# Optimization experiments

Hardware: AMD Instinct MI355X
Metric: run time of the kernel (lower is better)

The kernel has to match this reference:

```python
import jax, jax.numpy as jnp
import numpy as np

TEMPERATURE = 0.1
NEGATIVE_WEIGHT = 1.0
NORM_EPS = 1e-12  # matches torch F.normalize clamp_min eps


def setup_inputs() -> dict:
    key = jax.random.key(0)
    x = jax.random.normal(key, (8, 128, 16, 8, 8), dtype=jnp.float32)
    return {"x": x}


def reference(x):
    B, F, T, H, W = x.shape
    # transpose(0,1).flatten(1).transpose(0,1): (B,F,T,H,W) -> (N, F), N = B*T*H*W
    feats = jnp.transpose(x, (1, 0, 2, 3, 4)).reshape(F, -1).T  # [N, F]
    norms = jnp.maximum(jnp.linalg.norm(feats, axis=1, keepdims=True), NORM_EPS)
    x_norm = feats / norms  # unit vectors, [N, F]
    sims = (x_norm @ x_norm.T) / TEMPERATURE  # [N, N] cosine similarities
    n = sims.shape[0]
    # masked_select(~eye) + logsumexp == logsumexp with diagonal set to -inf
    sims = jnp.where(jnp.eye(n, dtype=bool), -jnp.inf, sims)
    diversity_loss = jax.nn.logsumexp(sims)
    return NEGATIVE_WEIGHT * diversity_loss
```

## Files before the change

### kernel.cpp

```cpp
#include <hip/hip_runtime.h>
#include <hip/hip_fp8.h>
#include <math.h>


#define NTILE 8256
#define NPBLK 1376

typedef __attribute__((ext_vector_type(4))) float f32x4;
typedef __attribute__((ext_vector_type(2))) long i64x2;

#if __has_builtin(__builtin_amdgcn_exp2f)
#define EXP2F(x) __builtin_amdgcn_exp2f(x)
#else
#define EXP2F(x) exp2f(x)
#endif

__device__ inline unsigned int pk_fp8(float f0, float f1, float f2, float f3) {
#if __has_builtin(__builtin_amdgcn_cvt_pk_fp8_f32)
    unsigned int r = 0;
    r = __builtin_amdgcn_cvt_pk_fp8_f32(f0, f1, r, false);
    r = __builtin_amdgcn_cvt_pk_fp8_f32(f2, f3, r, true);
    return r;
#else
    union { unsigned char b[4]; unsigned int u; } v;
    v.b[0] = __hip_fp8_e4m3(f0).__x; v.b[1] = __hip_fp8_e4m3(f1).__x;
    v.b[2] = __hip_fp8_e4m3(f2).__x; v.b[3] = __hip_fp8_e4m3(f3).__x;
    return v.u;
#endif
}

__global__ __launch_bounds__(256)
void normalize_kernel(const float* __restrict__ x, unsigned char* __restrict__ Xs) {
    __shared__ float ldsf[128][33];
    __shared__ float ssred[8][32];
    __shared__ float invs[32];
    const int tid = threadIdx.x;
    const int b  = blockIdx.x >> 5;
    const int r0 = (blockIdx.x & 31) * 32;
    const int rl = tid & 31, fp = tid >> 5;
    const float* px = x + b * 131072 + r0 + rl;
    float ss = 0.f;
#pragma unroll
    for (int j = 0; j < 16; ++j) {
        int f = fp * 16 + j;
        float v = px[f * 1024];
        ldsf[f][rl] = v;
        ss = fmaf(v, v, ss);
    }
    ssred[fp][rl] = ss;
    __syncthreads();
    if (tid < 32) {
        float s = 0.f;
#pragma unroll
        for (int k = 0; k < 8; ++k) s += ssred[k][tid];
        invs[tid] = 1.0f / fmaxf(sqrtf(s), 1e-12f);
    }
    __syncthreads();
    {
        const int c   = tid;
        const int rgl = c >> 7;
        const int cc  = c & 127;
        const int t8  = (cc >> 6) & 1, q = (cc >> 4) & 3, r = cc & 15;
        const int row = rgl * 16 + r;
        const float inv = invs[row];
        union { unsigned int w[4]; int4 v; } u;
#pragma unroll
        for (int half = 0; half < 2; ++half) {
            const int k0 = t8 * 64 + half * 32 + q * 8;
            u.w[half * 2 + 0] = pk_fp8(ldsf[k0 + 0][row] * inv, ldsf[k0 + 1][row] * inv,
                                       ldsf[k0 + 2][row] * inv, ldsf[k0 + 3][row] * inv);
            u.w[half * 2 + 1] = pk_fp8(ldsf[k0 + 4][row] * inv, ldsf[k0 + 5][row] * inv,
                                       ldsf[k0 + 6][row] * inv, ldsf[k0 + 7][row] * inv);
        }
        const int rgg = blockIdx.x * 2 + rgl;
        ((int4*)Xs)[rgg * 128 + cc] = u.v;
    }
}

__global__ __launch_bounds__(256)
void gram_lse_kernel(const i64x2* __restrict__ Xs, float* __restrict__ partials) {
    const int bk = blockIdx.x;
    const int tid = threadIdx.x;
    const int lane = tid & 63, w = tid >> 6;
    const int ga = (w & 1) * 2;
    const int gb = (w >> 1) * 2;
    const int quad = lane >> 4, colL = lane & 15;
    const float C = 14.426950408889634f;

    int L = bk * 6, I0 = 0;
    while (L >= 128 - I0) { L -= 128 - I0; ++I0; }
    int Is[6], Js[6];
    {
        int ii = I0, jj = I0 + L;
#pragma unroll
        for (int s = 0; s < 6; ++s) {
            Is[s] = ii; Js[s] = jj;
            if (++jj == 128) { ++ii; jj = ii; }
        }
    }

    i64x2 av[2][2];
    int IcurA = Is[0];
#pragma unroll
    for (int g = 0; g < 2; ++g)
#pragma unroll
        for (int t8 = 0; t8 < 2; ++t8)
            av[g][t8] = Xs[(Is[0] * 4 + ga + g) * 128 + t8 * 64 + lane];

    float wsum = 0.f;
#pragma unroll
    for (int s = 0; s < 6; ++s) {
        if (Is[s] != IcurA) {
#pragma unroll
            for (int g = 0; g < 2; ++g)
#pragma unroll
                for (int t8 = 0; t8 < 2; ++t8)
                    av[g][t8] = Xs[(Is[s] * 4 + ga + g) * 128 + t8 * 64 + lane];
            IcurA = Is[s];
        }

        i64x2 bv[2][2];
#pragma unroll
        for (int g = 0; g < 2; ++g)
#pragma unroll
            for (int t8 = 0; t8 < 2; ++t8)
                bv[g][t8] = Xs[(Js[s] * 4 + gb + g) * 128 + t8 * 64 + lane];

        f32x4 acc[2][2];
#pragma unroll
        for (int i = 0; i < 2; ++i)
#pragma unroll
            for (int j = 0; j < 2; ++j) acc[i][j] = (f32x4){0.f, 0.f, 0.f, 0.f};
#pragma unroll
        for (int t = 0; t < 4; ++t) {
            const int th = t >> 1, tl = t & 1;
            long aL[2], bL[2];
#pragma unroll
            for (int g = 0; g < 2; ++g) {
                aL[g] = av[g][th][tl];
                bL[g] = bv[g][th][tl];
            }
#pragma unroll
            for (int i = 0; i < 2; ++i)
#pragma unroll
                for (int j = 0; j < 2; ++j)
                    acc[i][j] = __builtin_amdgcn_mfma_f32_16x16x32_fp8_fp8(
                        aL[i], bL[j], acc[i][j], 0, 0, 0);
        }

        const bool diagT = (Is[s] == Js[s]);
        float lsum = 0.f;
#pragma unroll
        for (int i = 0; i < 2; ++i) {
            const int rbase = (ga + i) * 16 + quad * 4;
#pragma unroll
            for (int j = 0; j < 2; ++j) {
                const int cbase = (gb + j) * 16 + colL;
#pragma unroll
                for (int g = 0; g < 4; ++g) {
                    if (diagT && (rbase + g == cbase)) continue;
                    lsum += EXP2F(fmaf(C, acc[i][j][g], -C));
                }
            }
        }
        wsum += diagT ? lsum : 2.0f * lsum;
    }

#pragma unroll
    for (int o = 32; o > 0; o >>= 1) wsum += __shfl_down(wsum, o, 64);
    __shared__ float red[4];
    if (lane == 0) red[w] = wsum;
    __syncthreads();
    if (tid == 0) partials[bk] = red[0] + red[1] + red[2] + red[3];
}

__global__ __launch_bounds__(256)
void final_kernel(const float* __restrict__ partials, float* __restrict__ out) {
    double s = 0.0;
    for (int i = threadIdx.x; i < NPBLK; i += 256) s += (double)partials[i];
#pragma unroll
    for (int o = 32; o > 0; o >>= 1) s += __shfl_down(s, o, 64);
    __shared__ double red[4];
    if ((threadIdx.x & 63) == 0) red[threadIdx.x >> 6] = s;
    __syncthreads();
    if (threadIdx.x == 0)
        out[0] = (float)(10.0 + log(red[0] + red[1] + red[2] + red[3]));
}

extern "C" void kernel_launch(void* const* d_in, const int* in_sizes, int n_in,
                              void* d_out, int out_size, void* d_ws, size_t ws_size,
                              hipStream_t stream) {
    const float* x = (const float*)d_in[0];
    float* out = (float*)d_out;
    float* partials = (float*)d_ws;
    unsigned char* Xs = (unsigned char*)d_ws + 131072;

    normalize_kernel<<<256, 256, 0, stream>>>(x, Xs);
    gram_lse_kernel<<<NPBLK, 256, 0, stream>>>((const i64x2*)Xs, partials);
    final_kernel<<<1, 256, 0, stream>>>(partials, out);
}
```

Before: 72.76 us.

## Stage 128-row macro tile pairs in LDS and reuse across 2x2 sub-tiles

Result: faster. 70.27 us (-3.4%).

```diff
diff --git a/kernel.cpp b/kernel.cpp
--- a/kernel.cpp
+++ b/kernel.cpp
@@ -3,8 +3,7 @@
 #include <math.h>
 
 
-#define NTILE 8256
-#define NPBLK 1376
+#define NMACR 2080
 
 typedef __attribute__((ext_vector_type(4))) float f32x4;
 typedef __attribute__((ext_vector_type(2))) long i64x2;
@@ -87,83 +86,99 @@
     const int quad = lane >> 4, colL = lane & 15;
     const float C = 14.426950408889634f;
 
-    int L = bk * 6, I0 = 0;
-    while (L >= 128 - I0) { L -= 128 - I0; ++I0; }
-    int Is[6], Js[6];
+    int I;
     {
-        int ii = I0, jj = I0 + L;
-#pragma unroll
-        for (int s = 0; s < 6; ++s) {
-            Is[s] = ii; Js[s] = jj;
-            if (++jj == 128) { ++ii; jj = ii; }
+        const int t = bk;
+        I = (int)((129.0 - sqrt(16641.0 - 8.0 * (double)t)) * 0.5);
+        if (I < 0) I = 0;
+        while ((((I + 1) * (128 - I)) >> 1) <= t) ++I;
+        while (((I * (129 - I)) >> 1) > t) --I;
+    }
+    const int J = I + (bk - ((I * (129 - I)) >> 1));
+    const bool diagM = (I == J);
+
+    __shared__ i64x2 ldsA[1024];
+    __shared__ i64x2 ldsB[1024];
+    {
+        const i64x2* pa = Xs + I * 1024;
+        if (diagM) {
+#pragma unroll
+            for (int i = 0; i < 4; ++i)
+                ldsA[tid + i * 256] = pa[tid + i * 256];
+        } else {
+            const i64x2* pb = Xs + J * 1024;
+#pragma unroll
+            for (int i = 0; i < 4; ++i) {
+                ldsA[tid + i * 256] = pa[tid + i * 256];
+                ldsB[tid + i * 256] = pb[tid + i * 256];
+            }
         }
     }
-
-    i64x2 av[2][2];
-    int IcurA = Is[0];
-#pragma unroll
-    for (int g = 0; g < 2; ++g)
-#pragma unroll
-        for (int t8 = 0; t8 < 2; ++t8)
-            av[g][t8] = Xs[(Is[0] * 4 + ga + g) * 128 + t8 * 64 + lane];
+    __syncthreads();
+    const i64x2* lb = diagM ? ldsA : ldsB;
+
+    i64x2 avv[2][2][2];
+#pragma unroll
+    for (int ti = 0; ti < 2; ++ti)
+#pragma unroll
+        for (int g = 0; g < 2; ++g)
+#pragma unroll
+            for (int t8 = 0; t8 < 2; ++t8)
+                avv[ti][g][t8] = ldsA[(ti * 4 + ga + g) * 128 + t8 * 64 + lane];
 
     float wsum = 0.f;
 #pragma unroll
-    for (int s = 0; s < 6; ++s) {
-        if (Is[s] != IcurA) {
-#pragma unroll
-            for (int g = 0; g < 2; ++g)
-#pragma unroll
-                for (int t8 = 0; t8 < 2; ++t8)
-                    av[g][t8] = Xs[(Is[s] * 4 + ga + g) * 128 + t8 * 64 + lane];
-            IcurA = Is[s];
-        }
-
-        i64x2 bv[2][2];
+    for (int tj = 0; tj < 2; ++tj) {
+        i64x2 bvv[2][2];
 #pragma unroll
         for (int g = 0; g < 2; ++g)
 #pragma unroll
             for (int t8 = 0; t8 < 2; ++t8)
-                bv[g][t8] = Xs[(Js[s] * 4 + gb + g) * 128 + t8 * 64 + lane];
-
-        f32x4 acc[2][2];
-#pragma unroll
-        for (int i = 0; i < 2; ++i)
-#pragma unroll
-            for (int j = 0; j < 2; ++j) acc[i][j] = (f32x4){0.f, 0.f, 0.f, 0.f};
-#pragma unroll
-        for (int t = 0; t < 4; ++t) {
-            const int th = t >> 1, tl = t & 1;
-            long aL[2], bL[2];
-#pragma unroll
-            for (int g = 0; g < 2; ++g) {
-                aL[g] = av[g][th][tl];
-                bL[g] = bv[g][th][tl];
+                bvv[g][t8] = lb[(tj * 4 + gb + g) * 128 + t8 * 64 + lane];
+
+#pragma unroll
+        for (int ti = 0; ti < 2; ++ti) {
+            if (diagM && ti > tj) continue;
+            const bool dsub = diagM && (ti == tj);
+
+            f32x4 acc[2][2];
+#pragma unroll
+            for (int i = 0; i < 2; ++i)
+#pragma unroll
+                for (int j = 0; j < 2; ++j) acc[i][j] = (f32x4){0.f, 0.f, 0.f, 0.f};
+#pragma unroll
+            for (int t = 0; t < 4; ++t) {
+                const int th = t >> 1, tl = t & 1;
+                long aL[2], bL[2];
+#pragma unroll
+                for (int g = 0; g < 2; ++g) {
+                    aL[g] = avv[ti][g][th][tl];
+                    bL[g] = bvv[g][th][tl];
+                }
+#pragma unroll
+                for (int i = 0; i < 2; ++i)
+#pragma unroll
+                    for (int j = 0; j < 2; ++j)
+                        acc[i][j] = __builtin_amdgcn_mfma_f32_16x16x32_fp8_fp8(
+                            aL[i], bL[j], acc[i][j], 0, 0, 0);
             }
-#pragma unroll
-            for (int i = 0; i < 2; ++i)
-#pragma unroll
-                for (int j = 0; j < 2; ++j)
-                    acc[i][j] = __builtin_amdgcn_mfma_f32_16x16x32_fp8_fp8(
-                        aL[i], bL[j], acc[i][j], 0, 0, 0);
-        }
-
-        const bool diagT = (Is[s] == Js[s]);
-        float lsum = 0.f;
-#pragma unroll
-        for (int i = 0; i < 2; ++i) {
-            const int rbase = (ga + i) * 16 + quad * 4;
-#pragma unroll
-            for (int j = 0; j < 2; ++j) {
-                const int cbase = (gb + j) * 16 + colL;
-#pragma unroll
-                for (int g = 0; g < 4; ++g) {
-                    if (diagT && (rbase + g == cbase)) continue;
-                    lsum += EXP2F(fmaf(C, acc[i][j][g], -C));
+
+            float lsum = 0.f;
+#pragma unroll
+            for (int i = 0; i < 2; ++i) {
+                const int rbase = (ga + i) * 16 + quad * 4;
+#pragma unroll
+                for (int j = 0; j < 2; ++j) {
+                    const int cbase = (gb + j) * 16 + colL;
+#pragma unroll
+                    for (int g = 0; g < 4; ++g) {
+                        if (dsub && (rbase + g == cbase)) continue;
+                        lsum += EXP2F(fmaf(C, acc[i][j][g], -C));
+                    }
                 }
             }
+            wsum += dsub ? lsum : 2.0f * lsum;
         }
-        wsum += diagT ? lsum : 2.0f * lsum;
     }
 
 #pragma unroll
@@ -177,7 +192,7 @@
 __global__ __launch_bounds__(256)
 void final_kernel(const float* __restrict__ partials, float* __restrict__ out) {
     double s = 0.0;
-    for (int i = threadIdx.x; i < NPBLK; i += 256) s += (double)partials[i];
+    for (int i = threadIdx.x; i < NMACR; i += 256) s += (double)partials[i];
 #pragma unroll
     for (int o = 32; o > 0; o >>= 1) s += __shfl_down(s, o, 64);
     __shared__ double red[4];
@@ -196,6 +211,6 @@
     unsigned char* Xs = (unsigned char*)d_ws + 131072;
 
     normalize_kernel<<<256, 256, 0, stream>>>(x, Xs);
-    gram_lse_kernel<<<NPBLK, 256, 0, stream>>>((const i64x2*)Xs, partials);
+    gram_lse_kernel<<<NMACR, 256, 0, stream>>>((const i64x2*)Xs, partials);
     final_kernel<<<1, 256, 0, stream>>>(partials, out);
 }
```
